# Kernel optimization log

Hardware: AMD Instinct MI355X
Metric: run time of the kernel (lower is better)

## Reference

```python
import jax, jax.numpy as jnp
import numpy as np

EPS = 1e-5


def batchnorm(x, gamma, beta):
    # training-mode BN over (N, T, V) per channel, biased variance (matches torch BN forward)
    mean = x.mean(axis=(0, 2, 3), keepdims=True)
    var = x.var(axis=(0, 2, 3), keepdims=True)
    return (x - mean) * jax.lax.rsqrt(var + EPS) * gamma[None, :, None, None] + beta[None, :, None, None]


def temporal_shift(x, shift, stride):
    # Per-channel learnable fractional temporal shift with linear interpolation,
    # zero padding outside [0, T) (reconstruction of Shift-GCN's CUDA shift op).
    N, C, T, V = x.shape
    Tout = T // stride
    pos = jnp.arange(Tout, dtype=x.dtype)[None, :] * stride + shift[:, None]  # (C, Tout)
    i0 = jnp.floor(pos).astype(jnp.int32)
    frac = pos - i0.astype(x.dtype)
    i1 = i0 + 1
    w0 = ((i0 >= 0) & (i0 < T)).astype(x.dtype) * (1.0 - frac)  # (C, Tout)
    w1 = ((i1 >= 0) & (i1 < T)).astype(x.dtype) * frac
    i0c = jnp.clip(i0, 0, T - 1)
    i1c = jnp.clip(i1, 0, T - 1)
    cidx = jnp.arange(C)[:, None]
    x0 = x[:, cidx, i0c]  # (N, C, Tout, V) gather along time per channel
    x1 = x[:, cidx, i1c]
    return x0 * w0[None, :, :, None] + x1 * w1[None, :, :, None]


def setup_inputs() -> dict:
    key = jax.random.key(0)
    ks = jax.random.split(key, 10)
    N, C, T, V = 64, 128, 300, 25
    D = 256  # out_channels
    R = C // 4  # SE reduction
    inp = {
        "x": jax.random.normal(ks[0], (N, C, T, V), dtype=jnp.float32),
        "epoch": 100,
        "bn1_gamma": jnp.ones((C,), jnp.float32),
        "bn1_beta": jnp.zeros((C,), jnp.float32),
        "bn2_gamma": jnp.ones((D,), jnp.float32),
        "bn2_beta": jnp.zeros((D,), jnp.float32),
        "shift_in_param": jax.random.uniform(ks[1], (C,), jnp.float32, -1.0, 1.0),
        "shift_out_param": jax.random.uniform(ks[2], (D,), jnp.float32, -1.0, 1.0),
        "fc1_w": jax.random.normal(ks[3], (R, C), jnp.float32) * (1.0 / np.sqrt(C)),
        "fc1_b": jnp.zeros((R,), jnp.float32),
        "fc2_w": jax.random.normal(ks[4], (4, R), jnp.float32) * (1.0 / np.sqrt(R)),
        "fc2_b": jnp.zeros((4,), jnp.float32),
        "temporal_weight": jax.random.normal(ks[5], (4, C, D), jnp.float32) * np.sqrt(1.0 / D),
        "temporal_bias": jnp.zeros((4, D), jnp.float32),
    }
    return inp


def reference(x, epoch, bn1_gamma, bn1_beta, bn2_gamma, bn2_beta,
              shift_in_param, shift_out_param, fc1_w, fc1_b, fc2_w, fc2_b,
              temporal_weight, temporal_bias):
    x = batchnorm(x, bn1_gamma, bn1_beta)
    x = temporal_shift(x, shift_in_param, 1)
    # DY_SEModule: global avg pool -> 1x1 convs -> temperature softmax gate over 4 branches
    p = x.mean(axis=(2, 3))  # (N, C)
    h = jax.nn.relu(p @ fc1_w.T + fc1_b)
    logits = h @ fc2_w.T + fc2_b  # (N, 4)
    tao = (-(30.0 - 1.0) / 60.0 * epoch + 30.0) if epoch < 60 else 1.0
    gate = jax.nn.softmax(logits / tao, axis=1)  # (N, 4)
    w = jnp.einsum('kcd,nk->ncd', temporal_weight, gate)  # per-sample dynamic weight
    b = jnp.einsum('kc,nk->nc', temporal_bias, gate)
    x = jnp.einsum('nctv,ncd->ndtv', x, w) + b[:, :, None, None]
    x = jax.nn.relu(x)
    x = temporal_shift(x, shift_out_param, 1)  # stride=1
    x = batchnorm(x, bn2_gamma, bn2_beta)
    return x
```

## Files before the change

kernel.cpp:

```cpp
#include <hip/hip_runtime.h>
#include <stdint.h>

#define NN 64
#define CC 128
#define TT 300
#define VV 25
#define TV 7500
#define DD 256
#define RR 32
#define JPAD 7552
#define JT 125
#define NJT 60
#define XSTR 181
#define CBL 32
#define ZSTR 136

#define OFF_S1P    0
#define OFF_SS1P   8192
#define OFF_PS     16384
#define OFF_A1     24576
#define OFF_B1     24704
#define OFF_SUM2   24832
#define OFF_SUMSQ2 25088
#define OFF_GATE   25856
#define OFF_BIAS2  26112
#define OFF_CORR0  42496
#define OFF_CORR9  58880
#define FLOAT_REGION 75264
#define ZERO_CNT   25344
#define WT_BYTE_OFF ((size_t)FLOAT_REGION * 4)
#define WT_BYTES    ((size_t)NN * DD * CC * 2)
#define Z_BYTE_OFF  (WT_BYTE_OFF + WT_BYTES)

typedef __attribute__((ext_vector_type(8))) short short8;
typedef __attribute__((ext_vector_type(4))) float f32x4;

typedef const __attribute__((address_space(1))) uint32_t gas_u32;
typedef __attribute__((address_space(3))) uint32_t las_u32;

__device__ inline ushort f2bf(float f) {
    uint32_t u = __float_as_uint(f);
    u += 0x7fffu + ((u >> 16) & 1u);
    return (ushort)(u >> 16);
}
__device__ inline float bf2f(ushort v) { return __uint_as_float(((uint32_t)v) << 16); }
__device__ inline void async_copy16(const void* g, void* l) {
    __builtin_amdgcn_global_load_lds((gas_u32*)g, (las_u32*)l, 16, 0, 0);
}

__device__ inline void block_reduce2(float& a, float& b) {
    __shared__ float sa[4], sb[4];
    for (int off = 32; off > 0; off >>= 1) {
        a += __shfl_down(a, off);
        b += __shfl_down(b, off);
    }
    int lane = threadIdx.x & 63, wid = threadIdx.x >> 6;
    if (lane == 0) { sa[wid] = a; sb[wid] = b; }
    __syncthreads();
    if (threadIdx.x == 0) {
        a = sa[0] + sa[1] + sa[2] + sa[3];
        b = sb[0] + sb[1] + sb[2] + sb[3];
    }
}

__global__ void k_zero(float* ws) {
    int i = blockIdx.x * 256 + threadIdx.x;
    for (; i < ZERO_CNT; i += 32 * 256) ws[i] = 0.f;
}

__global__ __launch_bounds__(256) void k_shift_stats(const float* __restrict__ x,
                                                     const float* __restrict__ shift_in,
                                                     float* __restrict__ ws,
                                                     ushort* __restrict__ yT) {
    __shared__ float  xw[CBL * XSTR];
    __shared__ ushort ytile[CBL * 128];
    int jt = blockIdx.x, ch = blockIdx.y, n = blockIdx.z;
    int j0 = jt * JT;
    int t0 = jt * 5;
    int t_lo = max(t0 - 1, 0);
    int start_f = (t_lo * VV) & ~3;
    int doff = t_lo * VV - start_f;
    int tid = threadIdx.x;
    int lane = tid & 63, w = tid >> 6;
    int nvalid = min(45, (TV - start_f) >> 2);

    const float* xbase = x + ((size_t)n * CC + ch * CBL) * TV;
#pragma unroll
    for (int rr = 0; rr < 8; ++rr) {
        int cl = w * 8 + rr;
        if (lane < nvalid) {
            float4 u = *(const float4*)(xbase + (size_t)cl * TV + start_f + lane * 4);
            int b = cl * XSTR + lane * 4;
            xw[b] = u.x; xw[b + 1] = u.y; xw[b + 2] = u.z; xw[b + 3] = u.w;
        }
    }
    __syncthreads();

    int k = tid & 7;
    int cl = tid >> 3;
    int c = ch * CBL + cl;
    float sh = shift_in[c];
    bool posi = (sh >= 0.f);
    float asv = fabsf(sh);
    float wt = 1.f - asv;
    const float* xrow = &xw[cl * XSTR];
    int tapK = (t0 - t_lo) * VV + doff;
    int ntK  = posi ? (tapK + VV) : (tapK - VV);
    int wmax = (jt == NJT - 1) ? (TV - start_f - 1) : (7 * VV + doff - 1);
    bool eLo = (jt == 0) && !posi;
    bool eHi = (jt == NJT - 1) && posi;
    int key = (cl & 7) ^ ((cl >> 3) & 7);
    float s_p = 0.f, s_x = 0.f, s_xx = 0.f;
    int jbase = k * 16;
    ushort pk[16];
#pragma unroll
    for (int e = 0; e < 16; ++e) {
        int jtl = jbase + e;
        int ja = min(jtl, JT - 1);
        float xv = xrow[ja + tapK];
        int np = min(max(ja + ntK, 0), wmax);
        float ot = xrow[np];
        float wn = asv;
        if (eLo && jtl < VV) wn = 0.f;
        if (eHi && jtl >= JT - VV) wn = 0.f;
        float yv = wt * xv + wn * ot;
        bool valid = jtl < JT;
        yv = valid ? yv : 0.f;
        float xs = valid ? xv : 0.f;
        s_p += yv; s_x += xs; s_xx += xs * xs;
        pk[e] = f2bf(yv);
    }
    for (int off = 4; off > 0; off >>= 1) {
        s_p += __shfl_down(s_p, off, 8);
        s_x += __shfl_down(s_x, off, 8);
        s_xx += __shfl_down(s_xx, off, 8);
    }
    if (k == 0) {
        atomicAdd(&ws[OFF_PS + n * CC + c], s_p);
        atomicAdd(&ws[OFF_S1P + c * 64 + n], s_x);
        atomicAdd(&ws[OFF_SS1P + c * 64 + n], s_xx);
    }
#pragma unroll
    for (int h2 = 0; h2 < 2; ++h2) {
        uint32_t d0 = (uint32_t)pk[h2 * 8 + 0] | ((uint32_t)pk[h2 * 8 + 1] << 16);
        uint32_t d1 = (uint32_t)pk[h2 * 8 + 2] | ((uint32_t)pk[h2 * 8 + 3] << 16);
        uint32_t d2 = (uint32_t)pk[h2 * 8 + 4] | ((uint32_t)pk[h2 * 8 + 5] << 16);
        uint32_t d3 = (uint32_t)pk[h2 * 8 + 6] | ((uint32_t)pk[h2 * 8 + 7] << 16);
        int ci = 2 * k + h2;
        int m = (ci & 8) + ((ci & 7) ^ key);
        uint4 v; v.x = d0; v.y = d1; v.z = d2; v.w = d3;
        *(uint4*)&ytile[cl * 128 + m * 8] = v;
    }
    __syncthreads();

    for (int it = 0; it < 2; ++it) {
        int idx = it * 256 + tid;
        int s = idx & 3;
        int jl = idx >> 2;
        if (jl < JT) {
            int p = jl >> 6, jqv = (jl >> 3) & 7, e = jl & 7;
            uint32_t dw[4];
#pragma unroll
            for (int h = 0; h < 4; ++h) {
                int c0 = 8 * s + 2 * h, c1 = c0 + 1;
                int m0 = p * 8 + (jqv ^ (c0 & 7) ^ s);
                int m1 = p * 8 + (jqv ^ (c1 & 7) ^ s);
                ushort lo = ytile[c0 * 128 + m0 * 8 + e];
                ushort hi = ytile[c1 * 128 + m1 * 8 + e];
                dw[h] = (uint32_t)lo | ((uint32_t)hi << 16);
            }
            int jg = j0 + jl;
            int sg = ch * 4 + s;
            size_t rowb = ((size_t)n * JPAD + jg) * 128;
            *(uint4*)&yT[rowb + (size_t)((sg ^ (jg & 7)) << 3)] = *(uint4*)dw;
        }
    }
}

__global__ void k_gate(const float* __restrict__ g1, const float* __restrict__ b1,
                       const float* __restrict__ fc1_w, const float* __restrict__ fc1_b,
                       const float* __restrict__ fc2_w, const float* __restrict__ fc2_b,
                       const float* __restrict__ shift_in,
                       const int* __restrict__ epoch_p, float* ws) {
    __shared__ float psh[NN][CC];
    __shared__ float hsh[NN][RR];
    int tid = threadIdx.x;
    if (tid < CC) {
        int c = tid;
        float s = 0.f, ss = 0.f;
        for (int g = 0; g < 64; ++g) { s += ws[OFF_S1P + c * 64 + g]; ss += ws[OFF_SS1P + c * 64 + g]; }
        const float inv = 1.f / (float)(NN * TV);
        float m = s * inv;
        float var = ss * inv - m * m;
        float rstd = rsqrtf(var + 1e-5f);
        float A = rstd * g1[c];
        ws[OFF_A1 + c] = A;
        ws[OFF_B1 + c] = b1[c] - m * A;
    }
    __syncthreads();
    const float invTV = 1.f / (float)TV;
    for (int idx = tid; idx < NN * CC; idx += 256) {
        int n = idx >> 7, c = idx & 127;
        float sh = shift_in[c];
        float gb = (sh >= 0.f) ? (1.f - sh) : (1.f + sh);
        float meang = (299.f + gb) * (1.f / 300.f);
        psh[n][c] = ws[OFF_A1 + c] * (ws[OFF_PS + n * CC + c] * invTV) + ws[OFF_B1 + c] * meang;
    }
    __syncthreads();
    int n = tid >> 2;
    int rq = tid & 3;
    for (int r = rq * 8; r < rq * 8 + 8; ++r) {
        float acc = fc1_b[r];
        for (int c = 0; c < CC; ++c) acc += psh[n][c] * fc1_w[r * CC + c];
        hsh[n][r] = fmaxf(acc, 0.f);
    }
    __syncthreads();
    if (tid < NN) {
        int nn = tid;
        int ep = *epoch_p;
        float tao = (ep < 60) ? (-(29.f / 60.f) * (float)ep + 30.f) : 1.f;
        float li[4];
        float mx = -1e30f;
        for (int k = 0; k < 4; ++k) {
            float acc = fc2_b[k];
            for (int r = 0; r < RR; ++r) acc += hsh[nn][r] * fc2_w[k * RR + r];
            li[k] = acc / tao;
            mx = fmaxf(mx, li[k]);
        }
        float se = 0.f;
        for (int k = 0; k < 4; ++k) { li[k] = expf(li[k] - mx); se += li[k]; }
        float inv = 1.f / se;
        for (int k = 0; k < 4; ++k) ws[OFF_GATE + nn * 4 + k] = li[k] * inv;
    }
}

__global__ __launch_bounds__(256) void k_wmix(const float* __restrict__ tw, const float* __restrict__ tb,
                                              const float* __restrict__ shift_in,
                                              float* __restrict__ ws, ushort* __restrict__ wT) {
    int n = blockIdx.x, d = threadIdx.x;
    const float* g = &ws[OFF_GATE + n * 4];
    float g0 = g[0], g1 = g[1], g2 = g[2], g3 = g[3];
    float bias2 = g0 * tb[d] + g1 * tb[DD + d] + g2 * tb[2 * DD + d] + g3 * tb[3 * DD + d];
    float c0acc = 0.f, c9acc = 0.f;
    ushort* wrow = wT + ((size_t)n * DD + d) * 128;
    for (int s = 0; s < 16; ++s) {
        uint32_t dw[4];
#pragma unroll
        for (int h = 0; h < 4; ++h) {
            ushort e01[2];
#pragma unroll
            for (int q = 0; q < 2; ++q) {
                int c = s * 8 + 2 * h + q;
                const float* twc = tw + (size_t)c * DD + d;
                float wv = g0 * twc[0] + g1 * twc[32768] + g2 * twc[65536] + g3 * twc[98304];
                float A = ws[OFF_A1 + c], B = ws[OFF_B1 + c];
                float sh = shift_in[c];
                bias2 += B * wv;
                if (sh >= 0.f) c9acc += B * sh * wv; else c0acc += B * (-sh) * wv;
                e01[q] = f2bf(A * wv);
            }
            dw[h] = (uint32_t)e01[0] | ((uint32_t)e01[1] << 16);
        }
        *(uint4*)&wrow[(s ^ (d & 7)) << 3] = *(uint4*)dw;
    }
    ws[OFF_BIAS2 + n * DD + d] = bias2;
    ws[OFF_CORR0 + n * DD + d] = c0acc;
    ws[OFF_CORR9 + n * DD + d] = c9acc;
}

__global__ __launch_bounds__(256, 2) void k_gemm(const ushort* __restrict__ yT,
                                                 const ushort* __restrict__ wT,
                                                 const float* __restrict__ ws,
                                                 ushort* __restrict__ zbuf) {
    __shared__ char smem[65536];
    ushort* yl  = (ushort*)smem;
    ushort* zst = (ushort*)smem;
    ushort* wlb[2] = { (ushort*)(smem + 32768), (ushort*)(smem + 49152) };
    int jt = blockIdx.x, n = blockIdx.y;
    int tid = threadIdx.x;
    const char* ysrc = (const char*)(yT + ((size_t)n * JPAD + jt * 128) * 128);
    const char* wsrc = (const char*)(wT + (size_t)n * DD * 128);
#pragma unroll
    for (int i = 0; i < 8; ++i)
        async_copy16(ysrc + (size_t)(i * 256 + tid) * 16, (char*)yl + (i * 256 + tid) * 16);
#pragma unroll
    for (int i = 0; i < 4; ++i)
        async_copy16(wsrc + (size_t)(i * 256 + tid) * 16, (char*)wlb[0] + (i * 256 + tid) * 16);
    __syncthreads();
    int lane = tid & 63, wid = tid >> 6;
    int wm = wid >> 1, wn = wid & 1;
    int l16 = lane & 15, g = lane >> 4;
    bool edge = (jt == 0) || (jt == 58);
    short8 bfr[4][4];
#pragma unroll
    for (int ni = 0; ni < 4; ++ni)
#pragma unroll
        for (int ks = 0; ks < 4; ++ks) {
            int chunk = (ks * 4 + g) ^ (l16 & 7);
            bfr[ni][ks] = *(const short8*)&yl[(wn * 64 + ni * 16 + l16) * 128 + chunk * 8];
        }
    __syncthreads();
#pragma unroll
    for (int dt = 0; dt < 4; ++dt) {
        if (dt < 3) {
            const char* wc = wsrc + (size_t)(dt + 1) * 16384;
#pragma unroll
            for (int i = 0; i < 4; ++i)
                async_copy16(wc + (size_t)(i * 256 + tid) * 16,
                             (char*)wlb[(dt + 1) & 1] + (i * 256 + tid) * 16);
        }
        const ushort* wcur = wlb[dt & 1];
        f32x4 acc[2][4];
#pragma unroll
        for (int a = 0; a < 2; ++a)
#pragma unroll
            for (int b = 0; b < 4; ++b) acc[a][b] = (f32x4)0.f;
#pragma unroll
        for (int ks = 0; ks < 4; ++ks) {
            short8 af[2];
            int chunk = (ks * 4 + g) ^ (l16 & 7);
#pragma unroll
            for (int mi = 0; mi < 2; ++mi)
                af[mi] = *(const short8*)&wcur[(wm * 32 + mi * 16 + l16) * 128 + chunk * 8];
#pragma unroll
            for (int mi = 0; mi < 2; ++mi)
#pragma unroll
                for (int ni = 0; ni < 4; ++ni)
                    acc[mi][ni] = __builtin_amdgcn_mfma_f32_16x16x32_bf16(af[mi], bfr[ni][ks], acc[mi][ni], 0, 0, 0);
        }
#pragma unroll
        for (int mi = 0; mi < 2; ++mi) {
#pragma unroll
            for (int r = 0; r < 4; ++r) {
                int dl = wm * 32 + mi * 16 + g * 4 + r;
                int d = dt * 64 + dl;
                float bias = ws[OFF_BIAS2 + n * DD + d];
                float cr0 = 0.f, cr9 = 0.f;
                if (edge) { cr0 = ws[OFF_CORR0 + n * DD + d]; cr9 = ws[OFF_CORR9 + n * DD + d]; }
#pragma unroll
                for (int ni = 0; ni < 4; ++ni) {
                    int jl = wn * 64 + ni * 16 + l16;
                    float pre = acc[mi][ni][r] + bias;
                    if (edge) {
                        int jg = jt * 128 + jl;
                        if (jg < VV) pre -= cr0;
                        if (jg >= TV - VV) pre -= cr9;
                    }
                    zst[dl * ZSTR + jl] = f2bf(fmaxf(pre, 0.f));
                }
            }
        }
        __syncthreads();
#pragma unroll
        for (int it = 0; it < 4; ++it) {
            int idx = it * 256 + tid;
            int row = idx >> 4, q = idx & 15;
            uint4 v = *(const uint4*)&zst[row * ZSTR + q * 8];
            *(uint4*)&zbuf[((size_t)n * DD + dt * 64 + row) * JPAD + jt * 128 + q * 8] = v;
        }
        __syncthreads();
    }
}

__global__ __launch_bounds__(256) void k_bn2_stats(const ushort* __restrict__ zbuf,
                                                   const float* __restrict__ shift_out,
                                                   float* __restrict__ ws) {
    __shared__ ushort zl[JPAD];
    int d = blockIdx.x & 255;
    int n = blockIdx.x >> 8;
    int tid = threadIdx.x;
    const char* zrow = (const char*)(zbuf + ((size_t)n * DD + d) * JPAD);
    for (int k = tid; k < JPAD / 8; k += 256)
        async_copy16(zrow + (size_t)k * 16, (char*)zl + k * 16);
    __syncthreads();
    float sh = shift_out[d];
    float alpha = (sh >= 0.f) ? (1.f - sh) : (-sh);
    float beta  = (sh >= 0.f) ? sh : (1.f + sh);
    int o25 = (sh >= 0.f) ? 0 : -25;
    float s = 0.f, ss = 0.f;
    for (int jj = tid; jj < TV; jj += 256) {
        int i0 = jj + o25, i1 = jj + o25 + 25;
        float z0 = bf2f(zl[max(i0, 0)]);
        float z1 = bf2f(zl[min(i1, TV - 1)]);
        z0 = (i0 >= 0) ? z0 : 0.f;
        z1 = (i1 < TV) ? z1 : 0.f;
        float zs = alpha * z0 + beta * z1;
        s += zs;
        ss += zs * zs;
    }
    block_reduce2(s, ss);
    if (tid == 0) {
        atomicAdd(&ws[OFF_SUM2 + d], s);
        atomicAdd(&ws[OFF_SUMSQ2 + d], ss);
    }
}

__global__ __launch_bounds__(256) void k_out(const ushort* __restrict__ zbuf,
                                             const float* __restrict__ shift_out,
                                             const float* __restrict__ g2,
                                             const float* __restrict__ b2,
                                             const float* __restrict__ ws,
                                             float* __restrict__ out) {
    __shared__ ushort zl[JPAD];
    int d = blockIdx.x & 255;
    int n = blockIdx.x >> 8;
    int tid = threadIdx.x;
    const char* zrow = (const char*)(zbuf + ((size_t)n * DD + d) * JPAD);
    for (int k = tid; k < JPAD / 8; k += 256)
        async_copy16(zrow + (size_t)k * 16, (char*)zl + k * 16);
    const float inv = 1.f / (float)(NN * TV);
    float m = ws[OFF_SUM2 + d] * inv;
    float var = ws[OFF_SUMSQ2 + d] * inv - m * m;
    float rstd = rsqrtf(var + 1e-5f);
    float A = rstd * g2[d];
    float B = b2[d] - m * A;
    __syncthreads();
    float sh = shift_out[d];
    float alpha = (sh >= 0.f) ? (1.f - sh) : (-sh);
    float beta  = (sh >= 0.f) ? sh : (1.f + sh);
    int o25 = (sh >= 0.f) ? 0 : -25;
    float4* orow = (float4*)(out + ((size_t)n * DD + d) * TV);
    for (int k = tid; k < TV / 4; k += 256) {
        int jj = k * 4;
        float4 o4;
        float* op = &o4.x;
#pragma unroll
        for (int q = 0; q < 4; ++q) {
            int i0 = jj + q + o25, i1 = jj + q + o25 + 25;
            float z0 = bf2f(zl[max(i0, 0)]);
            float z1 = bf2f(zl[min(i1, TV - 1)]);
            z0 = (i0 >= 0) ? z0 : 0.f;
            z1 = (i1 < TV) ? z1 : 0.f;
            op[q] = (alpha * z0 + beta * z1) * A + B;
        }
        orow[k] = o4;
    }
}

extern "C" void kernel_launch(void* const* d_in, const int* in_sizes, int n_in,
                              void* d_out, int out_size, void* d_ws, size_t ws_size,
                              hipStream_t stream) {
    const float* x        = (const float*)d_in[0];
    const int*   epoch    = (const int*)d_in[1];
    const float* bn1_g    = (const float*)d_in[2];
    const float* bn1_b    = (const float*)d_in[3];
    const float* bn2_g    = (const float*)d_in[4];
    const float* bn2_b    = (const float*)d_in[5];
    const float* shift_in = (const float*)d_in[6];
    const float* shift_out= (const float*)d_in[7];
    const float* fc1_w    = (const float*)d_in[8];
    const float* fc1_b    = (const float*)d_in[9];
    const float* fc2_w    = (const float*)d_in[10];
    const float* fc2_b    = (const float*)d_in[11];
    const float* tw       = (const float*)d_in[12];
    const float* tb       = (const float*)d_in[13];
    float* out = (float*)d_out;
    float* ws  = (float*)d_ws;
    ushort* yT = (ushort*)d_out;
    ushort* wT = (ushort*)((char*)d_ws + WT_BYTE_OFF);
    ushort* zb = (ushort*)((char*)d_ws + Z_BYTE_OFF);

    k_zero<<<32, 256, 0, stream>>>(ws);
    k_shift_stats<<<dim3(NJT, 4, NN), 256, 0, stream>>>(x, shift_in, ws, yT);
    k_gate<<<1, 256, 0, stream>>>(bn1_g, bn1_b, fc1_w, fc1_b, fc2_w, fc2_b, shift_in, epoch, ws);
    k_wmix<<<64, 256, 0, stream>>>(tw, tb, shift_in, ws, wT);
    k_gemm<<<dim3(59, 64), 256, 0, stream>>>(yT, wT, ws, zb);
    k_bn2_stats<<<16384, 256, 0, stream>>>(zb, shift_out, ws);
    k_out<<<16384, 256, 0, stream>>>(zb, shift_out, bn2_g, bn2_b, ws, out);
}
```

Before: 489.2 us.

## Fuse gate into weight-mix kernel and store GEMM output directly from registers

The single-block gate kernel is merged into the per-sample weight-mix kernel. Each of the 64 blocks now recomputes the BN1 coefficients and its own SE gate, which removes one launch and a serial one-block stage at the cost of some redundant work. The GEMM swaps its operand roles so each lane holds four consecutive time-vertex outputs. Those results are written straight to global memory as 8-byte stores, dropping the LDS staging buffer and two barriers per d-tile, but the global stores become narrower and more scattered.

```diff
diff --git a/kernel.cpp b/kernel.cpp
--- a/kernel.cpp
+++ b/kernel.cpp
@@ -13,13 +13,10 @@
 #define NJT 60
 #define XSTR 181
 #define CBL 32
-#define ZSTR 136
 
 #define OFF_S1P    0
 #define OFF_SS1P   8192
 #define OFF_PS     16384
-#define OFF_A1     24576
-#define OFF_B1     24704
 #define OFF_SUM2   24832
 #define OFF_SUMSQ2 25088
 #define OFF_GATE   25856
@@ -177,14 +174,15 @@
     }
 }
 
-__global__ void k_gate(const float* __restrict__ g1, const float* __restrict__ b1,
-                       const float* __restrict__ fc1_w, const float* __restrict__ fc1_b,
-                       const float* __restrict__ fc2_w, const float* __restrict__ fc2_b,
-                       const float* __restrict__ shift_in,
-                       const int* __restrict__ epoch_p, float* ws) {
-    __shared__ float psh[NN][CC];
-    __shared__ float hsh[NN][RR];
-    int tid = threadIdx.x;
+__global__ __launch_bounds__(256) void k_wmix(const float* __restrict__ g1, const float* __restrict__ b1,
+                                              const float* __restrict__ fc1_w, const float* __restrict__ fc1_b,
+                                              const float* __restrict__ fc2_w, const float* __restrict__ fc2_b,
+                                              const int* __restrict__ epoch_p,
+                                              const float* __restrict__ tw, const float* __restrict__ tb,
+                                              const float* __restrict__ shift_in,
+                                              float* __restrict__ ws, ushort* __restrict__ wT) {
+    __shared__ float A1s[CC], B1s[CC], psh[CC], hsh[RR], gsh[4];
+    int n = blockIdx.x, tid = threadIdx.x;
     if (tid < CC) {
         int c = tid;
         float s = 0.f, ss = 0.f;
@@ -192,55 +190,46 @@
         const float inv = 1.f / (float)(NN * TV);
         float m = s * inv;
         float var = ss * inv - m * m;
-        float rstd = rsqrtf(var + 1e-5f);
-        float A = rstd * g1[c];
-        ws[OFF_A1 + c] = A;
-        ws[OFF_B1 + c] = b1[c] - m * A;
-    }
-    __syncthreads();
-    const float invTV = 1.f / (float)TV;
-    for (int idx = tid; idx < NN * CC; idx += 256) {
-        int n = idx >> 7, c = idx & 127;
+        float A = rsqrtf(var + 1e-5f) * g1[c];
+        float B = b1[c] - m * A;
+        A1s[c] = A; B1s[c] = B;
         float sh = shift_in[c];
         float gb = (sh >= 0.f) ? (1.f - sh) : (1.f + sh);
         float meang = (299.f + gb) * (1.f / 300.f);
-        psh[n][c] = ws[OFF_A1 + c] * (ws[OFF_PS + n * CC + c] * invTV) + ws[OFF_B1 + c] * meang;
-    }
-    __syncthreads();
-    int n = tid >> 2;
-    int rq = tid & 3;
-    for (int r = rq * 8; r < rq * 8 + 8; ++r) {
-        float acc = fc1_b[r];
-        for (int c = 0; c < CC; ++c) acc += psh[n][c] * fc1_w[r * CC + c];
-        hsh[n][r] = fmaxf(acc, 0.f);
-    }
-    __syncthreads();
-    if (tid < NN) {
-        int nn = tid;
+        psh[c] = A * (ws[OFF_PS + n * CC + c] * (1.f / (float)TV)) + B * meang;
+    }
+    __syncthreads();
+    {
+        int r = tid >> 3, lane8 = tid & 7;
+        float acc = 0.f;
+        for (int c = lane8; c < CC; c += 8) acc += psh[c] * fc1_w[r * CC + c];
+        for (int off = 4; off > 0; off >>= 1) acc += __shfl_down(acc, off, 8);
+        if (lane8 == 0) hsh[r] = fmaxf(acc + fc1_b[r], 0.f);
+    }
+    __syncthreads();
+    if (tid == 0) {
         int ep = *epoch_p;
         float tao = (ep < 60) ? (-(29.f / 60.f) * (float)ep + 30.f) : 1.f;
         float li[4];
         float mx = -1e30f;
-        for (int k = 0; k < 4; ++k) {
-            float acc = fc2_b[k];
-            for (int r = 0; r < RR; ++r) acc += hsh[nn][r] * fc2_w[k * RR + r];
-            li[k] = acc / tao;
-            mx = fmaxf(mx, li[k]);
+#pragma unroll
+        for (int kk = 0; kk < 4; ++kk) {
+            float acc = fc2_b[kk];
+            for (int r = 0; r < RR; ++r) acc += hsh[r] * fc2_w[kk * RR + r];
+            li[kk] = acc / tao;
+            mx = fmaxf(mx, li[kk]);
         }
         float se = 0.f;
-        for (int k = 0; k < 4; ++k) { li[k] = expf(li[k] - mx); se += li[k]; }
+#pragma unroll
+        for (int kk = 0; kk < 4; ++kk) { li[kk] = expf(li[kk] - mx); se += li[kk]; }
         float inv = 1.f / se;
-        for (int k = 0; k < 4; ++k) ws[OFF_GATE + nn * 4 + k] = li[k] * inv;
-    }
-}
-
-__global__ __launch_bounds__(256) void k_wmix(const float* __restrict__ tw, const float* __restrict__ tb,
-                                              const float* __restrict__ shift_in,
-                                              float* __restrict__ ws, ushort* __restrict__ wT) {
-    int n = blockIdx.x, d = threadIdx.x;
-    const float* g = &ws[OFF_GATE + n * 4];
-    float g0 = g[0], g1 = g[1], g2 = g[2], g3 = g[3];
-    float bias2 = g0 * tb[d] + g1 * tb[DD + d] + g2 * tb[2 * DD + d] + g3 * tb[3 * DD + d];
+#pragma unroll
+        for (int kk = 0; kk < 4; ++kk) gsh[kk] = li[kk] * inv;
+    }
+    __syncthreads();
+    int d = tid;
+    float g0 = gsh[0], g1v = gsh[1], g2 = gsh[2], g3 = gsh[3];
+    float bias2 = g0 * tb[d] + g1v * tb[DD + d] + g2 * tb[2 * DD + d] + g3 * tb[3 * DD + d];
     float c0acc = 0.f, c9acc = 0.f;
     ushort* wrow = wT + ((size_t)n * DD + d) * 128;
     for (int s = 0; s < 16; ++s) {
@@ -252,8 +241,8 @@
             for (int q = 0; q < 2; ++q) {
                 int c = s * 8 + 2 * h + q;
                 const float* twc = tw + (size_t)c * DD + d;
-                float wv = g0 * twc[0] + g1 * twc[32768] + g2 * twc[65536] + g3 * twc[98304];
-                float A = ws[OFF_A1 + c], B = ws[OFF_B1 + c];
+                float wv = g0 * twc[0] + g1v * twc[32768] + g2 * twc[65536] + g3 * twc[98304];
+                float A = A1s[c], B = B1s[c];
                 float sh = shift_in[c];
                 bias2 += B * wv;
                 if (sh >= 0.f) c9acc += B * sh * wv; else c0acc += B * (-sh) * wv;
@@ -272,10 +261,8 @@
                                                  const ushort* __restrict__ wT,
                                                  const float* __restrict__ ws,
                                                  ushort* __restrict__ zbuf) {
-    __shared__ char smem[65536];
-    ushort* yl  = (ushort*)smem;
-    ushort* zst = (ushort*)smem;
-    ushort* wlb[2] = { (ushort*)(smem + 32768), (ushort*)(smem + 49152) };
+    __shared__ ushort yl[128 * 128];
+    __shared__ ushort wlb[2][64 * 128];
     int jt = blockIdx.x, n = blockIdx.y;
     int tid = threadIdx.x;
     const char* ysrc = (const char*)(yT + ((size_t)n * JPAD + jt * 128) * 128);
@@ -288,20 +275,20 @@
         async_copy16(wsrc + (size_t)(i * 256 + tid) * 16, (char*)wlb[0] + (i * 256 + tid) * 16);
     __syncthreads();
     int lane = tid & 63, wid = tid >> 6;
-    int wm = wid >> 1, wn = wid & 1;
+    int wj = wid >> 1, wd = wid & 1;
     int l16 = lane & 15, g = lane >> 4;
     bool edge = (jt == 0) || (jt == 58);
-    short8 bfr[4][4];
-#pragma unroll
-    for (int ni = 0; ni < 4; ++ni)
+    short8 yfr[4][4];
+#pragma unroll
+    for (int ji = 0; ji < 4; ++ji)
 #pragma unroll
         for (int ks = 0; ks < 4; ++ks) {
             int chunk = (ks * 4 + g) ^ (l16 & 7);
-            bfr[ni][ks] = *(const short8*)&yl[(wn * 64 + ni * 16 + l16) * 128 + chunk * 8];
-        }
-    __syncthreads();
+            yfr[ji][ks] = *(const short8*)&yl[(wj * 64 + ji * 16 + l16) * 128 + chunk * 8];
+        }
 #pragma unroll
     for (int dt = 0; dt < 4; ++dt) {
+        if (dt) __syncthreads();
         if (dt < 3) {
             const char* wc = wsrc + (size_t)(dt + 1) * 16384;
 #pragma unroll
@@ -310,55 +297,49 @@
                              (char*)wlb[(dt + 1) & 1] + (i * 256 + tid) * 16);
         }
         const ushort* wcur = wlb[dt & 1];
-        f32x4 acc[2][4];
-#pragma unroll
-        for (int a = 0; a < 2; ++a)
-#pragma unroll
-            for (int b = 0; b < 4; ++b) acc[a][b] = (f32x4)0.f;
+        f32x4 acc[4][2];
+#pragma unroll
+        for (int a = 0; a < 4; ++a)
+#pragma unroll
+            for (int b = 0; b < 2; ++b) acc[a][b] = (f32x4)0.f;
 #pragma unroll
         for (int ks = 0; ks < 4; ++ks) {
-            short8 af[2];
+            short8 wf[2];
             int chunk = (ks * 4 + g) ^ (l16 & 7);
 #pragma unroll
-            for (int mi = 0; mi < 2; ++mi)
-                af[mi] = *(const short8*)&wcur[(wm * 32 + mi * 16 + l16) * 128 + chunk * 8];
-#pragma unroll
-            for (int mi = 0; mi < 2; ++mi)
-#pragma unroll
-                for (int ni = 0; ni < 4; ++ni)
-                    acc[mi][ni] = __builtin_amdgcn_mfma_f32_16x16x32_bf16(af[mi], bfr[ni][ks], acc[mi][ni], 0, 0, 0);
-        }
-#pragma unroll
-        for (int mi = 0; mi < 2; ++mi) {
-#pragma unroll
-            for (int r = 0; r < 4; ++r) {
-                int dl = wm * 32 + mi * 16 + g * 4 + r;
-                int d = dt * 64 + dl;
-                float bias = ws[OFF_BIAS2 + n * DD + d];
-                float cr0 = 0.f, cr9 = 0.f;
-                if (edge) { cr0 = ws[OFF_CORR0 + n * DD + d]; cr9 = ws[OFF_CORR9 + n * DD + d]; }
-#pragma unroll
-                for (int ni = 0; ni < 4; ++ni) {
-                    int jl = wn * 64 + ni * 16 + l16;
-                    float pre = acc[mi][ni][r] + bias;
-                    if (edge) {
-                        int jg = jt * 128 + jl;
-                        if (jg < VV) pre -= cr0;
-                        if (jg >= TV - VV) pre -= cr9;
-                    }
-                    zst[dl * ZSTR + jl] = f2bf(fmaxf(pre, 0.f));
+            for (int di = 0; di < 2; ++di)
+                wf[di] = *(const short8*)&wcur[(wd * 32 + di * 16 + l16) * 128 + chunk * 8];
+#pragma unroll
+            for (int ji = 0; ji < 4; ++ji)
+#pragma unroll
+                for (int di = 0; di < 2; ++di)
+                    acc[ji][di] = __builtin_amdgcn_mfma_f32_16x16x32_bf16(yfr[ji][ks], wf[di], acc[ji][di], 0, 0, 0);
+        }
+#pragma unroll
+        for (int di = 0; di < 2; ++di) {
+            int d = dt * 64 + wd * 32 + di * 16 + l16;
+            float bias = ws[OFF_BIAS2 + n * DD + d];
+            float cr0 = 0.f, cr9 = 0.f;
+            if (edge) { cr0 = ws[OFF_CORR0 + n * DD + d]; cr9 = ws[OFF_CORR9 + n * DD + d]; }
+            size_t zrow = ((size_t)n * DD + d) * JPAD;
+#pragma unroll
+            for (int ji = 0; ji < 4; ++ji) {
+                int jl = wj * 64 + ji * 16 + g * 4;
+                f32x4 v = acc[ji][di];
+                float e0 = v[0] + bias, e1 = v[1] + bias, e2 = v[2] + bias, e3 = v[3] + bias;
+                if (edge) {
+                    int jg = jt * 128 + jl;
+                    if (jg + 0 < VV) e0 -= cr0;  if (jg + 0 >= TV - VV) e0 -= cr9;
+                    if (jg + 1 < VV) e1 -= cr0;  if (jg + 1 >= TV - VV) e1 -= cr9;
+                    if (jg + 2 < VV) e2 -= cr0;  if (jg + 2 >= TV - VV) e2 -= cr9;
+                    if (jg + 3 < VV) e3 -= cr0;  if (jg + 3 >= TV - VV) e3 -= cr9;
                 }
+                uint2 pv;
+                pv.x = (uint32_t)f2bf(fmaxf(e0, 0.f)) | ((uint32_t)f2bf(fmaxf(e1, 0.f)) << 16);
+                pv.y = (uint32_t)f2bf(fmaxf(e2, 0.f)) | ((uint32_t)f2bf(fmaxf(e3, 0.f)) << 16);
+                *(uint2*)&zbuf[zrow + jt * 128 + jl] = pv;
             }
         }
-        __syncthreads();
-#pragma unroll
-        for (int it = 0; it < 4; ++it) {
-            int idx = it * 256 + tid;
-            int row = idx >> 4, q = idx & 15;
-            uint4 v = *(const uint4*)&zst[row * ZSTR + q * 8];
-            *(uint4*)&zbuf[((size_t)n * DD + dt * 64 + row) * JPAD + jt * 128 + q * 8] = v;
-        }
-        __syncthreads();
     }
 }
 
@@ -462,8 +443,8 @@
 
     k_zero<<<32, 256, 0, stream>>>(ws);
     k_shift_stats<<<dim3(NJT, 4, NN), 256, 0, stream>>>(x, shift_in, ws, yT);
-    k_gate<<<1, 256, 0, stream>>>(bn1_g, bn1_b, fc1_w, fc1_b, fc2_w, fc2_b, shift_in, epoch, ws);
-    k_wmix<<<64, 256, 0, stream>>>(tw, tb, shift_in, ws, wT);
+    k_wmix<<<64, 256, 0, stream>>>(bn1_g, bn1_b, fc1_w, fc1_b, fc2_w, fc2_b, epoch,
+                                   tw, tb, shift_in, ws, wT);
     k_gemm<<<dim3(59, 64), 256, 0, stream>>>(yT, wT, ws, zb);
     k_bn2_stats<<<16384, 256, 0, stream>>>(zb, shift_out, ws);
     k_out<<<16384, 256, 0, stream>>>(zb, shift_out, bn2_g, bn2_b, ws, out);
```

After: 434.2 us. 11.2% less time.
